# Kernel optimization log

Hardware: AMD Instinct MI355X
Metric: run time of the kernel (lower is better)

## Reference

```python
import jax, jax.numpy as jnp
import numpy as np
import math

NUM_HEADS = 16


def setup_inputs() -> dict:
    key = jax.random.key(0)
    ks = jax.random.split(key, 5)
    B, C, H = 2, 2048, 1024
    return {
        "x": jax.random.normal(ks[0], (B, C, H), dtype=jnp.float32),
        "Wqkv_w": jax.random.normal(ks[1], (3 * H, H), dtype=jnp.float32) * (1.0 / math.sqrt(H)),
        "Wqkv_b": jax.random.normal(ks[2], (3 * H,), dtype=jnp.float32) * 0.02,
        "Wo_w": jax.random.normal(ks[3], (H, H), dtype=jnp.float32) * (1.0 / math.sqrt(H)),
        "Wo_b": jax.random.normal(ks[4], (H,), dtype=jnp.float32) * 0.02,
    }


def reference(x, Wqkv_w, Wqkv_b, Wo_w, Wo_b):
    B, C, H = x.shape
    nh = NUM_HEADS
    hd = H // nh
    # QKV projection (torch Linear: x @ W.T + b)
    qkv = x @ Wqkv_w.T + Wqkv_b                      # [B, C, 3H]
    qkv = qkv.reshape(B, C, 3, nh, hd)
    qkv = jnp.transpose(qkv, (2, 0, 3, 1, 4))        # [3, B, nh, C, hd]
    q, k, v = qkv[0], qkv[1], qkv[2]
    scale = 1.0 / math.sqrt(hd)
    att = jnp.einsum('bhqd,bhkd->bhqk', q, k) * scale  # [B, nh, C, C]
    causal = jnp.triu(jnp.ones((C, C), dtype=bool), k=1)  # True above diagonal
    att = jnp.where(causal[None, None], jnp.float32(-jnp.inf), att)
    att = jax.nn.softmax(att, axis=-1)
    # dropout p set to 0 (eval-mode math)
    out = jnp.einsum('bhqk,bhkd->bhqd', att, v)       # [B, nh, C, hd]
    out = jnp.transpose(out, (0, 2, 1, 3)).reshape(B, C, H)
    return out @ Wo_w.T + Wo_b
```

## Files before the change

kernel.cpp:

```cpp
#include <hip/hip_runtime.h>
#include <hip/hip_bf16.h>
#include <math.h>

typedef unsigned short u16;
typedef __attribute__((ext_vector_type(8))) __bf16 bf16x8;
typedef __attribute__((ext_vector_type(4))) float f32x4;
typedef __attribute__((ext_vector_type(8))) unsigned short u16x8;
typedef __attribute__((ext_vector_type(4))) unsigned int u32x4;

__device__ __forceinline__ u16 f2bf(float f) {
  union { float f; unsigned u; } x; x.f = f;
  unsigned r = x.u + 0x7fffu + ((x.u >> 16) & 1u);
  return (u16)(r >> 16);
}

__device__ __forceinline__ void gload16(const u16* g, u16* l) {
  __builtin_amdgcn_global_load_lds(
      (const __attribute__((address_space(1))) void*)g,
      (__attribute__((address_space(3))) void*)l, 16, 0, 0);
}

#define MFMA16(a, b, c) __builtin_amdgcn_mfma_f32_16x16x32_bf16((a), (b), (c), 0, 0, 0)

#define QSCALE 0.18033688011112043f

__global__ __launch_bounds__(256) void cast_all_kernel(
    const float* __restrict__ x, const float* __restrict__ wqkv,
    const float* __restrict__ wo, u16* __restrict__ xb,
    u16* __restrict__ wqb, u16* __restrict__ wob) {
  int i = blockIdx.x * 256 + threadIdx.x;
  const float* src; u16* dst;
  if (i < 1048576)      { src = x;    dst = xb;  }
  else if (i < 1835008) { src = wqkv; dst = wqb; i -= 1048576; }
  else                  { src = wo;   dst = wob; i -= 1835008; }
  f32x4 v = *(const f32x4*)(src + (size_t)i * 4);
  u16 o0 = f2bf(v[0]), o1 = f2bf(v[1]), o2 = f2bf(v[2]), o3 = f2bf(v[3]);
  unsigned lo = (unsigned)o0 | ((unsigned)o1 << 16);
  unsigned hi = (unsigned)o2 | ((unsigned)o3 << 16);
  ((unsigned*)dst)[(size_t)i * 2] = lo;
  ((unsigned*)dst)[(size_t)i * 2 + 1] = hi;
}

__device__ __forceinline__ void gemm_bt_128(
    const u16* __restrict__ A, const u16* __restrict__ B, int K, int m0, int n0,
    u16* As, u16* Bs, f32x4 acc[4][4]) {
  const int tid = threadIdx.x;
  const int lane = tid & 63;
  const int wr = tid >> 7;
  const int wc = (tid >> 6) & 1;
  for (int k0 = 0; k0 < K; k0 += 64) {
    #pragma unroll
    for (int it = 0; it < 4; ++it) {
      int c = it * 256 + tid;
      int row = c >> 3;
      int ko = (c & 7) << 3;
      gload16(A + (size_t)(m0 + row) * K + (k0 + ko), As + c * 8);
      gload16(B + (size_t)(n0 + row) * K + (k0 + ko), Bs + c * 8);
    }
    __syncthreads();
    #pragma unroll
    for (int kk = 0; kk < 2; ++kk) {
      bf16x8 a[4], b[4];
      #pragma unroll
      for (int m = 0; m < 4; ++m)
        a[m] = *(const bf16x8*)(As + ((wr * 64 + m * 16 + (lane & 15)) * 64 +
                                      kk * 32 + ((lane >> 4) << 3)));
      #pragma unroll
      for (int n = 0; n < 4; ++n)
        b[n] = *(const bf16x8*)(Bs + ((wc * 64 + n * 16 + (lane & 15)) * 64 +
                                      kk * 32 + ((lane >> 4) << 3)));
      #pragma unroll
      for (int m = 0; m < 4; ++m)
        #pragma unroll
        for (int n = 0; n < 4; ++n)
          acc[m][n] = MFMA16(a[m], b[n], acc[m][n]);
    }
    __syncthreads();
  }
}

__global__ __launch_bounds__(256) void gemm_qkv_kernel(
    const u16* __restrict__ X, const u16* __restrict__ W, const float* __restrict__ bias,
    u16* __restrict__ Qb, u16* __restrict__ Kb, u16* __restrict__ Vb) {
  __shared__ __align__(16) u16 S[17408];
  f32x4 acc[4][4];
  #pragma unroll
  for (int m = 0; m < 4; ++m)
    #pragma unroll
    for (int n = 0; n < 4; ++n) acc[m][n] = (f32x4){0.f, 0.f, 0.f, 0.f};
  const int m0 = blockIdx.y * 128;
  const int n0 = blockIdx.x * 128;
  gemm_bt_128(X, W, 1024, m0, n0, S, S + 8192, acc);

  const int tid = threadIdx.x;
  const int lane = tid & 63;
  const int wr = tid >> 7, wc = (tid >> 6) & 1;
  const int which = n0 >> 10;
  const float qs = (which == 0) ? QSCALE : 1.0f;
  u16* __restrict__ dst = (which == 0) ? Qb : (which == 1 ? Kb : Vb);

  #pragma unroll
  for (int m = 0; m < 4; ++m)
    #pragma unroll
    for (int n = 0; n < 4; ++n)
      #pragma unroll
      for (int j = 0; j < 4; ++j) {
        int row = wr * 64 + m * 16 + ((lane >> 4) << 2) + j;
        int col = wc * 64 + n * 16 + (lane & 15);
        float v = (acc[m][n][j] + bias[n0 + col]) * qs;
        S[row * 136 + col] = f2bf(v);
      }
  __syncthreads();

  #pragma unroll
  for (int i = 0; i < 8; ++i) {
    int c = i * 256 + tid;
    int row = c >> 4, ch = c & 15;
    u16x8 val = *(const u16x8*)(S + row * 136 + ch * 8);
    int grow = m0 + row;
    int bb = grow >> 11, q = grow & 2047;
    int gcol = n0 + ch * 8;
    int h = (gcol >> 6) & 15, d0 = gcol & 63;
    *(u16x8*)(dst + ((size_t)((bb * 16 + h) * 2048 + q)) * 64 + d0) = val;
  }
}

__global__ __launch_bounds__(256) void gemm_out_kernel(
    const u16* __restrict__ Ain, const u16* __restrict__ W, const float* __restrict__ bias,
    float* __restrict__ out) {
  __shared__ __align__(16) u16 As[64 * 64];
  __shared__ __align__(16) u16 Bs[128 * 64];
  const int tid = threadIdx.x;
  const int lane = tid & 63;
  const int wc = tid >> 6;
  const int m0 = blockIdx.y * 64;
  const int n0 = blockIdx.x * 128;
  f32x4 acc[4][2] = {};
  for (int k0 = 0; k0 < 1024; k0 += 64) {
    #pragma unroll
    for (int it = 0; it < 2; ++it) {
      int c = it * 256 + tid;
      gload16(Ain + (size_t)(m0 + (c >> 3)) * 1024 + k0 + ((c & 7) << 3), As + c * 8);
    }
    #pragma unroll
    for (int it = 0; it < 4; ++it) {
      int c = it * 256 + tid;
      gload16(W + (size_t)(n0 + (c >> 3)) * 1024 + k0 + ((c & 7) << 3), Bs + c * 8);
    }
    __syncthreads();
    #pragma unroll
    for (int kk = 0; kk < 2; ++kk) {
      bf16x8 a[4], b[2];
      #pragma unroll
      for (int m = 0; m < 4; ++m)
        a[m] = *(const bf16x8*)(As + ((m * 16 + (lane & 15)) * 64 +
                                      kk * 32 + ((lane >> 4) << 3)));
      #pragma unroll
      for (int n = 0; n < 2; ++n)
        b[n] = *(const bf16x8*)(Bs + ((wc * 32 + n * 16 + (lane & 15)) * 64 +
                                      kk * 32 + ((lane >> 4) << 3)));
      #pragma unroll
      for (int m = 0; m < 4; ++m)
        #pragma unroll
        for (int n = 0; n < 2; ++n)
          acc[m][n] = MFMA16(a[m], b[n], acc[m][n]);
    }
    __syncthreads();
  }
  #pragma unroll
  for (int m = 0; m < 4; ++m)
    #pragma unroll
    for (int n = 0; n < 2; ++n)
      #pragma unroll
      for (int j = 0; j < 4; ++j) {
        int row = m0 + m * 16 + ((lane >> 4) << 2) + j;
        int col = n0 + wc * 32 + n * 16 + (lane & 15);
        out[(size_t)row * 1024 + col] = acc[m][n][j] + bias[col];
      }
}

__device__ __forceinline__ void attn_one(
    const u16* __restrict__ Qh, const u16* __restrict__ Kh, const u16* __restrict__ Vh,
    u16* __restrict__ Ob, int bb, int h, int qt,
    u16 (*Ks)[64 * 64], u16 (*Vt)[64 * 64]) {
  const int tid = threadIdx.x, lane = tid & 63, w = tid >> 6;
  const int g = lane >> 4, q15 = lane & 15;

  bf16x8 qf[2];
  const int qrow = qt * 64 + w * 16 + q15;
  #pragma unroll
  for (int kk = 0; kk < 2; ++kk)
    qf[kk] = *(const bf16x8*)(Qh + (size_t)qrow * 64 + kk * 32 + g * 8);

  f32x4 acc_o[4];
  #pragma unroll
  for (int n = 0; n < 4; ++n) acc_o[n] = (f32x4){0.f, 0.f, 0.f, 0.f};
  float m_run = -INFINITY, l_run = 0.f;

  const int nt = qt + 1;

  auto stageK = [&](int t, int buf) {
    #pragma unroll
    for (int it = 0; it < 2; ++it) {
      int c = it * 256 + tid;
      int row = c >> 3, b8 = c & 7;
      gload16(Kh + (size_t)(t * 64 + row) * 64 + ((b8 ^ (row & 7)) << 3),
              Ks[buf] + c * 8);
    }
  };

  stageK(0, 0);
  #pragma unroll
  for (int it = 0; it < 2; ++it) {
    int kloc = it * 32 + (tid >> 3);
    int d0 = (tid & 7) << 3;
    u16x8 v = *(const u16x8*)(Vh + (size_t)kloc * 64 + d0);
    #pragma unroll
    for (int i = 0; i < 8; ++i) {
      int d = d0 + i;
      int fv = (d + (d >> 3)) & 7;
      Vt[0][d * 64 + (((kloc >> 3) ^ fv) << 3) + (kloc & 7)] = v[i];
    }
  }
  __syncthreads();

  for (int t = 0; t < nt; ++t) {
    const int cur = t & 1;
    const bool pre = (t + 1 < nt);
    u16x8 vreg[2];
    if (pre) {
      stageK(t + 1, cur ^ 1);
      #pragma unroll
      for (int it = 0; it < 2; ++it) {
        int kloc = it * 32 + (tid >> 3);
        int d0 = (tid & 7) << 3;
        vreg[it] = *(const u16x8*)(Vh + (size_t)((t + 1) * 64 + kloc) * 64 + d0);
      }
    }

    f32x4 accs[4];
    __builtin_amdgcn_s_setprio(1);
    #pragma unroll
    for (int cb = 0; cb < 4; ++cb) {
      accs[cb] = (f32x4){0.f, 0.f, 0.f, 0.f};
      #pragma unroll
      for (int kk = 0; kk < 2; ++kk) {
        int row = cb * 16 + q15;
        int kblk = kk * 4 + g;
        bf16x8 kf = *(const bf16x8*)(Ks[cur] + row * 64 + ((kblk ^ (row & 7)) << 3));
        accs[cb] = MFMA16(kf, qf[kk], accs[cb]);
      }
    }
    __builtin_amdgcn_s_setprio(0);
    if (t == nt - 1) {
      #pragma unroll
      for (int cb = 0; cb < 4; ++cb)
        #pragma unroll
        for (int j = 0; j < 4; ++j) {
          int kg = t * 64 + cb * 16 + 4 * g + j;
          if (kg > qrow) accs[cb][j] = -INFINITY;
        }
    }

    float mj = accs[0][0];
    #pragma unroll
    for (int cb = 0; cb < 4; ++cb)
      #pragma unroll
      for (int j = 0; j < 4; ++j) mj = fmaxf(mj, accs[cb][j]);
    mj = fmaxf(mj, __shfl_xor(mj, 16));
    mj = fmaxf(mj, __shfl_xor(mj, 32));
    if (!__all(mj - m_run <= 8.0f)) {
      float mn = fmaxf(m_run, mj);
      float sc = exp2f(m_run - mn);
      m_run = mn;
      l_run *= sc;
      float scj[4];
      #pragma unroll
      for (int j = 0; j < 4; ++j) scj[j] = __shfl(sc, 4 * g + j);
      #pragma unroll
      for (int n = 0; n < 4; ++n)
        #pragma unroll
        for (int j = 0; j < 4; ++j) acc_o[n][j] *= scj[j];
    }
    float rs = 0.f;
    #pragma unroll
    for (int cb = 0; cb < 4; ++cb)
      #pragma unroll
      for (int j = 0; j < 4; ++j) {
        float p = exp2f(accs[cb][j] - m_run);
        accs[cb][j] = p;
        rs += p;
      }
    rs += __shfl_xor(rs, 16);
    rs += __shfl_xor(rs, 32);
    l_run += rs;

    unsigned Wp[4][2];
    #pragma unroll
    for (int cb = 0; cb < 4; ++cb)
      #pragma unroll
      for (int hh = 0; hh < 2; ++hh)
        asm("v_cvt_pk_bf16_f32 %0, %1, %2"
            : "=v"(Wp[cb][hh]) : "v"(accs[cb][2 * hh]), "v"(accs[cb][2 * hh + 1]));

    unsigned aw[2][4];
    #pragma unroll
    for (int kk = 0; kk < 2; ++kk)
      #pragma unroll
      for (int iw = 0; iw < 4; ++iw) {
        int srcLane = q15 + ((((g & 1) << 1) + (iw >> 1)) << 4);
        unsigned c0 = __shfl(Wp[2 * kk + 0][iw & 1], srcLane);
        unsigned c1 = __shfl(Wp[2 * kk + 1][iw & 1], srcLane);
        aw[kk][iw] = (g >> 1) ? c1 : c0;
      }
    bf16x8 pa0 = __builtin_bit_cast(bf16x8, (u32x4){aw[0][0], aw[0][1], aw[0][2], aw[0][3]});
    bf16x8 pa1 = __builtin_bit_cast(bf16x8, (u32x4){aw[1][0], aw[1][1], aw[1][2], aw[1][3]});

    __builtin_amdgcn_s_setprio(1);
    #pragma unroll
    for (int n = 0; n < 4; ++n) {
      #pragma unroll
      for (int kk = 0; kk < 2; ++kk) {
        int cblk = kk * 4 + g;
        int d = n * 16 + q15;
        int fv = (d + (d >> 3)) & 7;
        bf16x8 vb = *(const bf16x8*)(Vt[cur] + d * 64 + ((cblk ^ fv) << 3));
        acc_o[n] = MFMA16(kk ? pa1 : pa0, vb, acc_o[n]);
      }
    }
    __builtin_amdgcn_s_setprio(0);

    if (pre) {
      #pragma unroll
      for (int it = 0; it < 2; ++it) {
        int kloc = it * 32 + (tid >> 3);
        int d0 = (tid & 7) << 3;
        #pragma unroll
        for (int i = 0; i < 8; ++i) {
          int d = d0 + i;
          int fv = (d + (d >> 3)) & 7;
          Vt[cur ^ 1][d * 64 + (((kloc >> 3) ^ fv) << 3) + (kloc & 7)] = vreg[it][i];
        }
      }
    }
    __syncthreads();
  }

  float invl = 1.0f / l_run;
  float invj[4];
  #pragma unroll
  for (int j = 0; j < 4; ++j) invj[j] = __shfl(invl, 4 * g + j);
  #pragma unroll
  for (int n = 0; n < 4; ++n)
    #pragma unroll
    for (int j = 0; j < 4; ++j) {
      int qg = qt * 64 + w * 16 + 4 * g + j;
      Ob[((size_t)(bb * 2048 + qg)) * 1024 + h * 64 + n * 16 + q15] =
          f2bf(acc_o[n][j] * invj[j]);
    }
}

__global__ __launch_bounds__(256, 4) void attn_kernel(
    const u16* __restrict__ Qb, const u16* __restrict__ Kb, const u16* __restrict__ Vb,
    u16* __restrict__ Ob) {
  __shared__ __align__(16) u16 Ks[2][64 * 64];
  __shared__ __align__(16) u16 Vt[2][64 * 64];
  const int blk = blockIdx.x;
  const int p = blk & 15;
  const int bh = blk >> 4;
  const size_t base = (size_t)bh * 2048 * 64;
  const int bb = bh >> 4, h = bh & 15;
  attn_one(Qb + base, Kb + base, Vb + base, Ob, bb, h, 31 - p, Ks, Vt);
  attn_one(Qb + base, Kb + base, Vb + base, Ob, bb, h, p, Ks, Vt);
}

extern "C" void kernel_launch(void* const* d_in, const int* in_sizes, int n_in,
                              void* d_out, int out_size, void* d_ws, size_t ws_size,
                              hipStream_t stream) {
  const float* x    = (const float*)d_in[0];
  const float* wqkv = (const float*)d_in[1];
  const float* bqkv = (const float*)d_in[2];
  const float* wo   = (const float*)d_in[3];
  const float* bo   = (const float*)d_in[4];
  float* out = (float*)d_out;

  const size_t MB = 1u << 20;
  char* ws = (char*)d_ws;
  u16* x_bf  = (u16*)(ws);
  u16* wq_bf = (u16*)(ws + 8 * MB);
  u16* wo_bf = (u16*)(ws + 14 * MB);
  u16* q_buf = (u16*)(ws + 16 * MB);
  u16* k_buf = (u16*)(ws + 24 * MB);
  u16* v_buf = (u16*)(ws + 32 * MB);
  u16* a_out = (u16*)(ws + 40 * MB);

  cast_all_kernel<<<8192, 256, 0, stream>>>(x, wqkv, wo, x_bf, wq_bf, wo_bf);

  gemm_qkv_kernel<<<dim3(24, 32), 256, 0, stream>>>(x_bf, wq_bf, bqkv,
                                                    q_buf, k_buf, v_buf);
  attn_kernel<<<512, 256, 0, stream>>>(q_buf, k_buf, v_buf, a_out);
  gemm_out_kernel<<<dim3(8, 64), 256, 0, stream>>>(a_out, wo_bf, bo, out);
}
```

Before: 147.7 us.

## Switch attention to 32x32 MFMA with 2-wave blocks and per-tile work scheduling

New measurement: 151.8 us. 1.03x slower.

```diff
diff --git a/kernel.cpp b/kernel.cpp
--- a/kernel.cpp
+++ b/kernel.cpp
@@ -5,8 +5,10 @@
 typedef unsigned short u16;
 typedef __attribute__((ext_vector_type(8))) __bf16 bf16x8;
 typedef __attribute__((ext_vector_type(4))) float f32x4;
+typedef __attribute__((ext_vector_type(16))) float f32x16;
 typedef __attribute__((ext_vector_type(8))) unsigned short u16x8;
 typedef __attribute__((ext_vector_type(4))) unsigned int u32x4;
+typedef __attribute__((ext_vector_type(2))) unsigned int u32x2;
 
 __device__ __forceinline__ u16 f2bf(float f) {
   union { float f; unsigned u; } x; x.f = f;
@@ -21,6 +23,7 @@
 }
 
 #define MFMA16(a, b, c) __builtin_amdgcn_mfma_f32_16x16x32_bf16((a), (b), (c), 0, 0, 0)
+#define MFMA32(a, b, c) __builtin_amdgcn_mfma_f32_32x32x16_bf16((a), (b), (c), 0, 0, 0)
 
 #define QSCALE 0.18033688011112043f
 
@@ -184,194 +187,178 @@
     u16* __restrict__ Ob, int bb, int h, int qt,
     u16 (*Ks)[64 * 64], u16 (*Vt)[64 * 64]) {
   const int tid = threadIdx.x, lane = tid & 63, w = tid >> 6;
-  const int g = lane >> 4, q15 = lane & 15;
-
-  bf16x8 qf[2];
-  const int qrow = qt * 64 + w * 16 + q15;
-  #pragma unroll
-  for (int kk = 0; kk < 2; ++kk)
-    qf[kk] = *(const bf16x8*)(Qh + (size_t)qrow * 64 + kk * 32 + g * 8);
-
-  f32x4 acc_o[4];
-  #pragma unroll
-  for (int n = 0; n < 4; ++n) acc_o[n] = (f32x4){0.f, 0.f, 0.f, 0.f};
+  const int half = lane >> 5, q31 = lane & 31;
+  const int qrow = qt * 64 + w * 32 + q31;
+
+  bf16x8 qf[4];
+  #pragma unroll
+  for (int ds = 0; ds < 4; ++ds)
+    qf[ds] = *(const bf16x8*)(Qh + (size_t)qrow * 64 + ds * 16 + half * 8);
+
+  f32x16 acc_o[2] = {};
   float m_run = -INFINITY, l_run = 0.f;
-
   const int nt = qt + 1;
 
   auto stageK = [&](int t, int buf) {
     #pragma unroll
-    for (int it = 0; it < 2; ++it) {
-      int c = it * 256 + tid;
+    for (int it = 0; it < 4; ++it) {
+      int c = it * 128 + tid;
       int row = c >> 3, b8 = c & 7;
       gload16(Kh + (size_t)(t * 64 + row) * 64 + ((b8 ^ (row & 7)) << 3),
               Ks[buf] + c * 8);
     }
   };
+  auto loadV = [&](int t, u16x8 vreg[4]) {
+    #pragma unroll
+    for (int it = 0; it < 4; ++it) {
+      int kloc = it * 16 + (tid >> 3);
+      int d0 = (tid & 7) << 3;
+      vreg[it] = *(const u16x8*)(Vh + (size_t)(t * 64 + kloc) * 64 + d0);
+    }
+  };
+  auto writeV = [&](const u16x8 vreg[4], int buf) {
+    #pragma unroll
+    for (int it = 0; it < 4; ++it) {
+      int kloc = it * 16 + (tid >> 3);
+      int d0 = (tid & 7) << 3;
+      #pragma unroll
+      for (int i = 0; i < 8; ++i) {
+        int d = d0 + i;
+        int fv = (d + (d >> 3)) & 7;
+        Vt[buf][d * 64 + (((kloc >> 3) ^ fv) << 3) + (kloc & 7)] = vreg[it][i];
+      }
+    }
+  };
 
   stageK(0, 0);
-  #pragma unroll
-  for (int it = 0; it < 2; ++it) {
-    int kloc = it * 32 + (tid >> 3);
-    int d0 = (tid & 7) << 3;
-    u16x8 v = *(const u16x8*)(Vh + (size_t)kloc * 64 + d0);
-    #pragma unroll
-    for (int i = 0; i < 8; ++i) {
-      int d = d0 + i;
-      int fv = (d + (d >> 3)) & 7;
-      Vt[0][d * 64 + (((kloc >> 3) ^ fv) << 3) + (kloc & 7)] = v[i];
-    }
+  {
+    u16x8 v0[4];
+    loadV(0, v0);
+    writeV(v0, 0);
   }
   __syncthreads();
 
   for (int t = 0; t < nt; ++t) {
     const int cur = t & 1;
     const bool pre = (t + 1 < nt);
-    u16x8 vreg[2];
-    if (pre) {
-      stageK(t + 1, cur ^ 1);
-      #pragma unroll
-      for (int it = 0; it < 2; ++it) {
-        int kloc = it * 32 + (tid >> 3);
-        int d0 = (tid & 7) << 3;
-        vreg[it] = *(const u16x8*)(Vh + (size_t)((t + 1) * 64 + kloc) * 64 + d0);
-      }
-    }
-
-    f32x4 accs[4];
+    u16x8 vreg[4];
+    if (pre) { stageK(t + 1, cur ^ 1); loadV(t + 1, vreg); }
+
+    f32x16 accs[2] = {};
     __builtin_amdgcn_s_setprio(1);
     #pragma unroll
-    for (int cb = 0; cb < 4; ++cb) {
-      accs[cb] = (f32x4){0.f, 0.f, 0.f, 0.f};
-      #pragma unroll
-      for (int kk = 0; kk < 2; ++kk) {
-        int row = cb * 16 + q15;
-        int kblk = kk * 4 + g;
-        bf16x8 kf = *(const bf16x8*)(Ks[cur] + row * 64 + ((kblk ^ (row & 7)) << 3));
-        accs[cb] = MFMA16(kf, qf[kk], accs[cb]);
+    for (int c = 0; c < 2; ++c) {
+      #pragma unroll
+      for (int ds = 0; ds < 4; ++ds) {
+        int row = c * 32 + q31;
+        int bi = 2 * ds + half;
+        bf16x8 kf = *(const bf16x8*)(Ks[cur] + row * 64 + ((bi ^ (row & 7)) << 3));
+        accs[c] = MFMA32(kf, qf[ds], accs[c]);
       }
     }
     __builtin_amdgcn_s_setprio(0);
+
     if (t == nt - 1) {
       #pragma unroll
-      for (int cb = 0; cb < 4; ++cb)
+      for (int c = 0; c < 2; ++c)
         #pragma unroll
-        for (int j = 0; j < 4; ++j) {
-          int kg = t * 64 + cb * 16 + 4 * g + j;
-          if (kg > qrow) accs[cb][j] = -INFINITY;
+        for (int r = 0; r < 16; ++r) {
+          int kg = t * 64 + c * 32 + (r & 3) + 8 * (r >> 2) + 4 * half;
+          if (kg > qrow) accs[c][r] = -INFINITY;
         }
     }
 
     float mj = accs[0][0];
     #pragma unroll
-    for (int cb = 0; cb < 4; ++cb)
-      #pragma unroll
-      for (int j = 0; j < 4; ++j) mj = fmaxf(mj, accs[cb][j]);
-    mj = fmaxf(mj, __shfl_xor(mj, 16));
+    for (int c = 0; c < 2; ++c)
+      #pragma unroll
+      for (int r = 0; r < 16; ++r) mj = fmaxf(mj, accs[c][r]);
     mj = fmaxf(mj, __shfl_xor(mj, 32));
     if (!__all(mj - m_run <= 8.0f)) {
       float mn = fmaxf(m_run, mj);
       float sc = exp2f(m_run - mn);
       m_run = mn;
       l_run *= sc;
-      float scj[4];
-      #pragma unroll
-      for (int j = 0; j < 4; ++j) scj[j] = __shfl(sc, 4 * g + j);
-      #pragma unroll
-      for (int n = 0; n < 4; ++n)
-        #pragma unroll
-        for (int j = 0; j < 4; ++j) acc_o[n][j] *= scj[j];
+      acc_o[0] *= sc;
+      acc_o[1] *= sc;
     }
     float rs = 0.f;
     #pragma unroll
-    for (int cb = 0; cb < 4; ++cb)
-      #pragma unroll
-      for (int j = 0; j < 4; ++j) {
-        float p = exp2f(accs[cb][j] - m_run);
-        accs[cb][j] = p;
+    for (int c = 0; c < 2; ++c)
+      #pragma unroll
+      for (int r = 0; r < 16; ++r) {
+        float p = exp2f(accs[c][r] - m_run);
+        accs[c][r] = p;
         rs += p;
       }
-    rs += __shfl_xor(rs, 16);
     rs += __shfl_xor(rs, 32);
     l_run += rs;
 
-    unsigned Wp[4][2];
-    #pragma unroll
-    for (int cb = 0; cb < 4; ++cb)
-      #pragma unroll
-      for (int hh = 0; hh < 2; ++hh)
+    unsigned Wp[2][8];
+    #pragma unroll
+    for (int c = 0; c < 2; ++c)
+      #pragma unroll
+      for (int m = 0; m < 8; ++m)
         asm("v_cvt_pk_bf16_f32 %0, %1, %2"
-            : "=v"(Wp[cb][hh]) : "v"(accs[cb][2 * hh]), "v"(accs[cb][2 * hh + 1]));
-
-    unsigned aw[2][4];
-    #pragma unroll
-    for (int kk = 0; kk < 2; ++kk)
-      #pragma unroll
-      for (int iw = 0; iw < 4; ++iw) {
-        int srcLane = q15 + ((((g & 1) << 1) + (iw >> 1)) << 4);
-        unsigned c0 = __shfl(Wp[2 * kk + 0][iw & 1], srcLane);
-        unsigned c1 = __shfl(Wp[2 * kk + 1][iw & 1], srcLane);
-        aw[kk][iw] = (g >> 1) ? c1 : c0;
-      }
-    bf16x8 pa0 = __builtin_bit_cast(bf16x8, (u32x4){aw[0][0], aw[0][1], aw[0][2], aw[0][3]});
-    bf16x8 pa1 = __builtin_bit_cast(bf16x8, (u32x4){aw[1][0], aw[1][1], aw[1][2], aw[1][3]});
-
-    __builtin_amdgcn_s_setprio(1);
-    #pragma unroll
-    for (int n = 0; n < 4; ++n) {
-      #pragma unroll
-      for (int kk = 0; kk < 2; ++kk) {
-        int cblk = kk * 4 + g;
-        int d = n * 16 + q15;
+            : "=v"(Wp[c][m]) : "v"(accs[c][2 * m]), "v"(accs[c][2 * m + 1]));
+
+    #pragma unroll
+    for (int k = 0; k < 4; ++k) {
+      const int c = k >> 1, g0 = 4 * (k & 1);
+      unsigned x0 = (unsigned)__shfl_xor((int)Wp[c][g0 + 0], 32);
+      unsigned x1 = (unsigned)__shfl_xor((int)Wp[c][g0 + 1], 32);
+      unsigned x2 = (unsigned)__shfl_xor((int)Wp[c][g0 + 2], 32);
+      unsigned x3 = (unsigned)__shfl_xor((int)Wp[c][g0 + 3], 32);
+      unsigned pa0 = half ? x2 : Wp[c][g0 + 0];
+      unsigned pa1 = half ? x3 : Wp[c][g0 + 1];
+      unsigned pa2 = half ? Wp[c][g0 + 2] : x0;
+      unsigned pa3 = half ? Wp[c][g0 + 3] : x1;
+      bf16x8 pb = __builtin_bit_cast(bf16x8, (u32x4){pa0, pa1, pa2, pa3});
+      __builtin_amdgcn_s_setprio(1);
+      #pragma unroll
+      for (int n = 0; n < 2; ++n) {
+        int d = n * 32 + q31;
         int fv = (d + (d >> 3)) & 7;
-        bf16x8 vb = *(const bf16x8*)(Vt[cur] + d * 64 + ((cblk ^ fv) << 3));
-        acc_o[n] = MFMA16(kk ? pa1 : pa0, vb, acc_o[n]);
-      }
-    }
-    __builtin_amdgcn_s_setprio(0);
-
-    if (pre) {
-      #pragma unroll
-      for (int it = 0; it < 2; ++it) {
-        int kloc = it * 32 + (tid >> 3);
-        int d0 = (tid & 7) << 3;
-        #pragma unroll
-        for (int i = 0; i < 8; ++i) {
-          int d = d0 + i;
-          int fv = (d + (d >> 3)) & 7;
-          Vt[cur ^ 1][d * 64 + (((kloc >> 3) ^ fv) << 3) + (kloc & 7)] = vreg[it][i];
-        }
-      }
-    }
+        int bi = 2 * k + half;
+        bf16x8 vfr = *(const bf16x8*)(Vt[cur] + d * 64 + ((bi ^ fv) << 3));
+        acc_o[n] = MFMA32(vfr, pb, acc_o[n]);
+      }
+      __builtin_amdgcn_s_setprio(0);
+    }
+
+    if (pre) writeV(vreg, cur ^ 1);
     __syncthreads();
   }
 
   float invl = 1.0f / l_run;
-  float invj[4];
-  #pragma unroll
-  for (int j = 0; j < 4; ++j) invj[j] = __shfl(invl, 4 * g + j);
-  #pragma unroll
-  for (int n = 0; n < 4; ++n)
-    #pragma unroll
-    for (int j = 0; j < 4; ++j) {
-      int qg = qt * 64 + w * 16 + 4 * g + j;
-      Ob[((size_t)(bb * 2048 + qg)) * 1024 + h * 64 + n * 16 + q15] =
-          f2bf(acc_o[n][j] * invj[j]);
-    }
-}
-
-__global__ __launch_bounds__(256, 4) void attn_kernel(
+  #pragma unroll
+  for (int n = 0; n < 2; ++n)
+    #pragma unroll
+    for (int rq = 0; rq < 4; ++rq) {
+      int dbase = n * 32 + 8 * rq + 4 * half;
+      u16 o0 = f2bf(acc_o[n][4 * rq + 0] * invl);
+      u16 o1 = f2bf(acc_o[n][4 * rq + 1] * invl);
+      u16 o2 = f2bf(acc_o[n][4 * rq + 2] * invl);
+      u16 o3 = f2bf(acc_o[n][4 * rq + 3] * invl);
+      unsigned lo = (unsigned)o0 | ((unsigned)o1 << 16);
+      unsigned hi = (unsigned)o2 | ((unsigned)o3 << 16);
+      size_t idx = ((size_t)(bb * 2048 + qrow)) * 1024 + h * 64 + dbase;
+      *(u32x2*)(Ob + idx) = (u32x2){lo, hi};
+    }
+}
+
+__global__ __launch_bounds__(128, 2) void attn_kernel(
     const u16* __restrict__ Qb, const u16* __restrict__ Kb, const u16* __restrict__ Vb,
     u16* __restrict__ Ob) {
   __shared__ __align__(16) u16 Ks[2][64 * 64];
   __shared__ __align__(16) u16 Vt[2][64 * 64];
-  const int blk = blockIdx.x;
-  const int p = blk & 15;
-  const int bh = blk >> 4;
+  const int b = blockIdx.x;
+  const int k = b >> 8, i = b & 255;
+  const int bh = i >> 3, j = i & 7;
+  const int qt = (k == 0) ? 2 * j : (k == 1) ? 2 * j + 1
+               : (k == 2) ? 31 - 2 * j : 30 - 2 * j;
   const size_t base = (size_t)bh * 2048 * 64;
-  const int bb = bh >> 4, h = bh & 15;
-  attn_one(Qb + base, Kb + base, Vb + base, Ob, bb, h, 31 - p, Ks, Vt);
-  attn_one(Qb + base, Kb + base, Vb + base, Ob, bb, h, p, Ks, Vt);
+  attn_one(Qb + base, Kb + base, Vb + base, Ob, bh >> 4, bh & 15, qt, Ks, Vt);
 }
 
 extern "C" void kernel_launch(void* const* d_in, const int* in_sizes, int n_in,
@@ -398,6 +385,6 @@
 
   gemm_qkv_kernel<<<dim3(24, 32), 256, 0, stream>>>(x_bf, wq_bf, bqkv,
                                                     q_buf, k_buf, v_buf);
-  attn_kernel<<<512, 256, 0, stream>>>(q_buf, k_buf, v_buf, a_out);
+  attn_kernel<<<1024, 128, 0, stream>>>(q_buf, k_buf, v_buf, a_out);
   gemm_out_kernel<<<dim3(8, 64), 256, 0, stream>>>(a_out, wo_bf, bo, out);
 }
```

## Rewrite QKV GEMM with 256x256 tiles, double-buffered async LDS prefetch and swizzle

Applied to the files above, without the earlier changes.

Measured after the change: 144.7 us. 2.1% less time.

```diff
diff --git a/kernel.cpp b/kernel.cpp
--- a/kernel.cpp
+++ b/kernel.cpp
@@ -41,87 +41,117 @@
   ((unsigned*)dst)[(size_t)i * 2 + 1] = hi;
 }
 
-__device__ __forceinline__ void gemm_bt_128(
-    const u16* __restrict__ A, const u16* __restrict__ B, int K, int m0, int n0,
-    u16* As, u16* Bs, f32x4 acc[4][4]) {
+__global__ __launch_bounds__(512, 2) void gemm_qkv_kernel(
+    const u16* __restrict__ X, const u16* __restrict__ W, const float* __restrict__ bias,
+    u16* __restrict__ Qb, u16* __restrict__ Kb, u16* __restrict__ Vb) {
+  __shared__ __align__(16) u16 As[2][2][128 * 64];
+  __shared__ __align__(16) u16 Bs[2][2][128 * 64];
   const int tid = threadIdx.x;
   const int lane = tid & 63;
-  const int wr = tid >> 7;
-  const int wc = (tid >> 6) & 1;
-  for (int k0 = 0; k0 < K; k0 += 64) {
-    #pragma unroll
-    for (int it = 0; it < 4; ++it) {
-      int c = it * 256 + tid;
-      int row = c >> 3;
-      int ko = (c & 7) << 3;
-      gload16(A + (size_t)(m0 + row) * K + (k0 + ko), As + c * 8);
-      gload16(B + (size_t)(n0 + row) * K + (k0 + ko), Bs + c * 8);
-    }
-    __syncthreads();
-    #pragma unroll
-    for (int kk = 0; kk < 2; ++kk) {
-      bf16x8 a[4], b[4];
-      #pragma unroll
-      for (int m = 0; m < 4; ++m)
-        a[m] = *(const bf16x8*)(As + ((wr * 64 + m * 16 + (lane & 15)) * 64 +
-                                      kk * 32 + ((lane >> 4) << 3)));
-      #pragma unroll
-      for (int n = 0; n < 4; ++n)
-        b[n] = *(const bf16x8*)(Bs + ((wc * 64 + n * 16 + (lane & 15)) * 64 +
-                                      kk * 32 + ((lane >> 4) << 3)));
-      #pragma unroll
-      for (int m = 0; m < 4; ++m)
+  const int wid = tid >> 6;
+  const int wm = wid >> 2, wn = wid & 3;
+  const int g = lane >> 4, q15 = lane & 15;
+  const int m0b = blockIdx.y * 256;
+  const int n0b = blockIdx.x * 256;
+  const int sA = 2 * ((q15 >> 2) & 1);
+
+  auto stageA = [&](int kt, int h) {
+    #pragma unroll
+    for (int it = 0; it < 2; ++it) {
+      int c = it * 512 + tid;
+      int row = c >> 3, kg = c & 7;
+      int kgs = kg ^ (2 * ((row >> 2) & 1));
+      gload16(X + (size_t)(m0b + h * 128 + row) * 1024 + kt * 64 + kgs * 8,
+              &As[kt & 1][h][c * 8]);
+    }
+  };
+  auto stageB = [&](int kt, int h) {
+    #pragma unroll
+    for (int it = 0; it < 2; ++it) {
+      int c = it * 512 + tid;
+      int row = c >> 3, kg = c & 7;
+      int kgs = kg ^ (2 * ((row >> 2) & 1));
+      gload16(W + (size_t)(n0b + h * 128 + row) * 1024 + kt * 64 + kgs * 8,
+              &Bs[kt & 1][h][c * 8]);
+    }
+  };
+
+  f32x4 acc[8][4] = {};
+
+  stageA(0, 0); stageA(0, 1);
+  stageB(0, 0); stageB(0, 1);
+  stageB(1, 0); stageB(1, 1);
+  asm volatile("s_waitcnt vmcnt(4)" ::: "memory");
+  __builtin_amdgcn_s_barrier();
+
+  for (int kt = 0; kt < 16; ++kt) {
+    const int d = kt & 1;
+    const u16* Ah = As[d][wm];
+    const u16* Bh = Bs[d][wn >> 1];
+    const int rB0 = (wn & 1) * 64;
+    bf16x8 bfr[4][2];
+    #pragma unroll
+    for (int q = 0; q < 4; ++q) {
+      bf16x8 afr[2][2];
+      if (q == 0) {
         #pragma unroll
         for (int n = 0; n < 4; ++n)
-          acc[m][n] = MFMA16(a[m], b[n], acc[m][n]);
-    }
-    __syncthreads();
+          #pragma unroll
+          for (int kk = 0; kk < 2; ++kk) {
+            int row = rB0 + n * 16 + q15;
+            int kg = (kk * 4 + g) ^ sA;
+            bfr[n][kk] = *(const bf16x8*)(Bh + row * 64 + kg * 8);
+          }
+      }
+      #pragma unroll
+      for (int p = 0; p < 2; ++p)
+        #pragma unroll
+        for (int kk = 0; kk < 2; ++kk) {
+          int row = (2 * q + p) * 16 + q15;
+          int kg = (kk * 4 + g) ^ sA;
+          afr[p][kk] = *(const bf16x8*)(Ah + row * 64 + kg * 8);
+        }
+      if (q == 0)      { if (kt + 1 < 16) stageA(kt + 1, 0); }
+      else if (q == 1) { if (kt + 1 < 16) stageA(kt + 1, 1); }
+      else if (q == 2) { if (kt + 2 < 16) stageB(kt + 2, 0); }
+      else             { if (kt + 2 < 16) stageB(kt + 2, 1); }
+      __builtin_amdgcn_s_barrier();
+      asm volatile("s_waitcnt lgkmcnt(0)" ::: "memory");
+      __builtin_amdgcn_sched_barrier(0);
+      __builtin_amdgcn_s_setprio(1);
+      #pragma unroll
+      for (int kk = 0; kk < 2; ++kk)
+        #pragma unroll
+        for (int p = 0; p < 2; ++p)
+          #pragma unroll
+          for (int n = 0; n < 4; ++n)
+            acc[2 * q + p][n] = MFMA16(afr[p][kk], bfr[n][kk], acc[2 * q + p][n]);
+      __builtin_amdgcn_s_setprio(0);
+      if (q == 3) {
+        if (kt < 14)       asm volatile("s_waitcnt vmcnt(4)" ::: "memory");
+        else if (kt == 14) asm volatile("s_waitcnt vmcnt(0)" ::: "memory");
+      }
+      __builtin_amdgcn_s_barrier();
+    }
   }
-}
-
-__global__ __launch_bounds__(256) void gemm_qkv_kernel(
-    const u16* __restrict__ X, const u16* __restrict__ W, const float* __restrict__ bias,
-    u16* __restrict__ Qb, u16* __restrict__ Kb, u16* __restrict__ Vb) {
-  __shared__ __align__(16) u16 S[17408];
-  f32x4 acc[4][4];
-  #pragma unroll
-  for (int m = 0; m < 4; ++m)
-    #pragma unroll
-    for (int n = 0; n < 4; ++n) acc[m][n] = (f32x4){0.f, 0.f, 0.f, 0.f};
-  const int m0 = blockIdx.y * 128;
-  const int n0 = blockIdx.x * 128;
-  gemm_bt_128(X, W, 1024, m0, n0, S, S + 8192, acc);
-
-  const int tid = threadIdx.x;
-  const int lane = tid & 63;
-  const int wr = tid >> 7, wc = (tid >> 6) & 1;
-  const int which = n0 >> 10;
+
+  const int which = n0b >> 10;
   const float qs = (which == 0) ? QSCALE : 1.0f;
   u16* __restrict__ dst = (which == 0) ? Qb : (which == 1 ? Kb : Vb);
-
-  #pragma unroll
-  for (int m = 0; m < 4; ++m)
-    #pragma unroll
-    for (int n = 0; n < 4; ++n)
+  #pragma unroll
+  for (int n = 0; n < 4; ++n) {
+    int gcol = n0b + wn * 64 + n * 16 + q15;
+    float bz = bias[gcol];
+    int h = (gcol >> 6) & 15, d0 = gcol & 63;
+    #pragma unroll
+    for (int m = 0; m < 8; ++m)
       #pragma unroll
       for (int j = 0; j < 4; ++j) {
-        int row = wr * 64 + m * 16 + ((lane >> 4) << 2) + j;
-        int col = wc * 64 + n * 16 + (lane & 15);
-        float v = (acc[m][n][j] + bias[n0 + col]) * qs;
-        S[row * 136 + col] = f2bf(v);
-      }
-  __syncthreads();
-
-  #pragma unroll
-  for (int i = 0; i < 8; ++i) {
-    int c = i * 256 + tid;
-    int row = c >> 4, ch = c & 15;
-    u16x8 val = *(const u16x8*)(S + row * 136 + ch * 8);
-    int grow = m0 + row;
-    int bb = grow >> 11, q = grow & 2047;
-    int gcol = n0 + ch * 8;
-    int h = (gcol >> 6) & 15, d0 = gcol & 63;
-    *(u16x8*)(dst + ((size_t)((bb * 16 + h) * 2048 + q)) * 64 + d0) = val;
+        int grow = m0b + wm * 128 + m * 16 + g * 4 + j;
+        int bb = grow >> 11, qq = grow & 2047;
+        dst[((size_t)((bb * 16 + h) * 2048 + qq)) * 64 + d0] =
+            f2bf((acc[m][n][j] + bz) * qs);
+      }
   }
 }
 
@@ -396,7 +426,7 @@
 
   cast_all_kernel<<<8192, 256, 0, stream>>>(x, wqkv, wo, x_bf, wq_bf, wo_bf);
 
-  gemm_qkv_kernel<<<dim3(24, 32), 256, 0, stream>>>(x_bf, wq_bf, bqkv,
+  gemm_qkv_kernel<<<dim3(12, 16), 512, 0, stream>>>(x_bf, wq_bf, bqkv,
                                                     q_buf, k_buf, v_buf);
   attn_kernel<<<512, 256, 0, stream>>>(q_buf, k_buf, v_buf, a_out);
   gemm_out_kernel<<<dim3(8, 64), 256, 0, stream>>>(a_out, wo_bf, bo, out);
```
